# Kernel optimization log

Hardware: AMD Instinct MI355X
Metric: run time of the kernel (lower is better)

Reference implementation:

```python
import jax, jax.numpy as jnp
import numpy as np

E = 1024   # embedding_size
H = 16     # num_heads
DH = E // H


def setup_inputs() -> dict:
    key = jax.random.key(0)
    ks = jax.random.split(key, 11)
    B, S = 2, 2048
    std = 0.02
    return {
        "query": jax.random.normal(ks[0], (B, S, E), jnp.float32),
        "key": jax.random.normal(ks[1], (B, S, E), jnp.float32),
        "value": jax.random.normal(ks[2], (B, S, E), jnp.float32),
        "Wq": jax.random.normal(ks[3], (E, E), jnp.float32) * std,
        "bq": jnp.zeros((E,), jnp.float32),
        "Wk": jax.random.normal(ks[4], (E, E), jnp.float32) * std,
        "bk": jnp.zeros((E,), jnp.float32),
        "Wv": jax.random.normal(ks[5], (E, E), jnp.float32) * std,
        "bv": jnp.zeros((E,), jnp.float32),
        "Wo": jax.random.normal(ks[6], (E, E), jnp.float32) * std,
        "bo": jnp.zeros((E,), jnp.float32),
    }


def _split_heads(x, B, S):
    # [B,S,E] -> [B,H,S,DH]
    return x.reshape(B, S, H, DH).transpose(0, 2, 1, 3)


def reference(query, key, value, Wq, bq, Wk, bk, Wv, bv, Wo, bo):
    B, S, _ = query.shape
    # torch Linear: y = x @ W.T + b
    q = _split_heads(query @ Wq.T + bq, B, S)
    k = _split_heads(key @ Wk.T + bk, B, key.shape[1])
    v = _split_heads(value @ Wv.T + bv, B, value.shape[1])
    # naive unscaled attention (original has no 1/sqrt(d) factor)
    scores = jnp.einsum("bhsd,bhtd->bhst", q, k)  # [B,H,S,T]
    attn = jax.nn.softmax(scores, axis=-1)
    out = jnp.einsum("bhst,bhtd->bhsd", attn, v)  # [B,H,S,DH]
    out = out.transpose(0, 2, 1, 3).reshape(B, S, E)
    return out @ Wo.T + bo
```

## Files before the change

kernel.cpp:

```cpp
#include <hip/hip_runtime.h>
#include <hip/hip_bf16.h>

constexpr int kB   = 2;
constexpr int kS   = 2048;
constexpr int kE   = 1024;
constexpr int kH   = 16;
constexpr int kDH  = 64;
constexpr int kTok = kB * kS;

typedef short bf16x8 __attribute__((ext_vector_type(8)));
typedef float f32x4  __attribute__((ext_vector_type(4)));

__device__ __forceinline__ float bf2f(unsigned short s) {
  union { unsigned int u; float f; } c; c.u = ((unsigned int)s) << 16; return c.f;
}
__device__ __forceinline__ unsigned short f2bf(float f) {
  union { float f; unsigned int u; } c; c.f = f;
  unsigned int u = c.u;
  u += 0x7fffu + ((u >> 16) & 1u);
  return (unsigned short)(u >> 16);
}

__device__ __forceinline__ void gl_lds16(const unsigned short* g, unsigned short* l) {
  __builtin_amdgcn_global_load_lds(
      (const __attribute__((address_space(1))) unsigned int*)g,
      (__attribute__((address_space(3))) unsigned int*)l, 16, 0, 0);
}

__global__ void detect_dtype(const unsigned short* __restrict__ q, int* flag) {
  __shared__ int cnt;
  if (threadIdx.x == 0) cnt = 0;
  __syncthreads();
  int bad = 0;
  for (int i = threadIdx.x; i < 4096; i += 256) {
    unsigned int e = (q[i] >> 7) & 0xFF;
    if (e >= 0xC0) bad++;
  }
  atomicAdd(&cnt, bad);
  __syncthreads();
  if (threadIdx.x == 0) *flag = (cnt > 8) ? 1 : 0;
}

struct Seg { const void* src; unsigned short* dst; unsigned int n; unsigned int blk0; };
struct ConvArgs { Seg s[11]; };

__global__ __launch_bounds__(256) void conv_all(ConvArgs a, const int* __restrict__ flag) {
  const unsigned int bid = blockIdx.x;
  int si = 0;
  #pragma unroll
  for (int i = 1; i < 11; ++i)
    if (bid >= a.s[i].blk0) si = i;
  const Seg sg = a.s[si];
  const int i0 = ((int)(bid - sg.blk0) * 256 + threadIdx.x) * 8;
  if (i0 >= (int)sg.n) return;
  if (*flag) {
    const float* s = (const float*)sg.src + i0;
    f32x4 f0 = *(const f32x4*)(s);
    f32x4 f1 = *(const f32x4*)(s + 4);
    bf16x8 v;
    #pragma unroll
    for (int j = 0; j < 4; ++j) v[j]     = (short)f2bf(f0[j]);
    #pragma unroll
    for (int j = 0; j < 4; ++j) v[j + 4] = (short)f2bf(f1[j]);
    *(bf16x8*)&sg.dst[i0] = v;
  } else {
    *(bf16x8*)&sg.dst[i0] = *(const bf16x8*)((const unsigned short*)sg.src + i0);
  }
}

__device__ __forceinline__ void gemm_core(
    const unsigned short* __restrict__ A,
    const unsigned short* __restrict__ W,
    int Kdim, int bM, int bN,
    unsigned short* As, unsigned short* Ws,
    f32x4 acc[4][4])
{
  const int tid  = threadIdx.x;
  const int lane = tid & 63;
  const int wv   = tid >> 6;
  const int wm   = (wv >> 1) * 64;
  const int wn   = (wv & 1) * 64;
  const int lr   = lane & 15;
  const int kq   = (lane >> 4) * 8;

  const int r0 = tid >> 2;
  const int c0 = (tid & 3) * 8;

  const unsigned short* Ag = A + (size_t)(bM + r0) * Kdim + c0;
  const unsigned short* Wg = W + (size_t)(bN + r0) * Kdim + c0;
  unsigned short* lA = &As[tid * 8];
  unsigned short* lW = &Ws[tid * 8];

  for (int k0 = 0; k0 < Kdim; k0 += 32) {
    gl_lds16(Ag + k0,                      lA);
    gl_lds16(Ag + (size_t)64 * Kdim + k0,  lA + 2048);
    gl_lds16(Wg + k0,                      lW);
    gl_lds16(Wg + (size_t)64 * Kdim + k0,  lW + 2048);
    __syncthreads();

    bf16x8 a[4], b[4];
    #pragma unroll
    for (int i = 0; i < 4; ++i)
      a[i] = *(const bf16x8*)&As[(wm + i * 16 + lr) * 32 + kq];
    #pragma unroll
    for (int i = 0; i < 4; ++i)
      b[i] = *(const bf16x8*)&Ws[(wn + i * 16 + lr) * 32 + kq];
    #pragma unroll
    for (int i = 0; i < 4; ++i)
      #pragma unroll
      for (int j = 0; j < 4; ++j)
        acc[i][j] = __builtin_amdgcn_mfma_f32_16x16x32_bf16(a[i], b[j], acc[i][j], 0, 0, 0);
    __syncthreads();
  }
}

__global__ __launch_bounds__(256) void gemm_qkv(
    const unsigned short* __restrict__ Abase,
    const unsigned short* __restrict__ Wbase,
    const unsigned short* __restrict__ biasbase,
    unsigned short* __restrict__ Cbase)
{
  __shared__ unsigned short As[128 * 32];
  __shared__ unsigned short Ws[128 * 32];

  const int z = blockIdx.z;
  const unsigned short* A    = Abase    + (size_t)z * (kTok * kE);
  const unsigned short* W    = Wbase    + (size_t)z * (kE * kE);
  const unsigned short* bias = biasbase + (size_t)z * kE;
  unsigned short* C          = Cbase    + (size_t)z * (kTok * kE);

  const int bM = blockIdx.y * 128;
  const int bN = blockIdx.x * 128;

  f32x4 acc[4][4] = {};
  gemm_core(A, W, kE, bM, bN, As, Ws, acc);

  const int lane = threadIdx.x & 63;
  const int wv   = threadIdx.x >> 6;
  const int wm   = (wv >> 1) * 64;
  const int wn   = (wv & 1) * 64;
  const int lr   = lane & 15;
  const int qd   = lane >> 4;
  #pragma unroll
  for (int j = 0; j < 4; ++j) {
    const int col = bN + wn + j * 16 + lr;
    const float bb = bf2f(bias[col]);
    #pragma unroll
    for (int i = 0; i < 4; ++i)
      #pragma unroll
      for (int r = 0; r < 4; ++r) {
        const int row = bM + wm + i * 16 + qd * 4 + r;
        C[(size_t)row * kE + col] = f2bf(acc[i][j][r] + bb);
      }
  }
}

__global__ __launch_bounds__(256) void vtrans(
    const unsigned short* __restrict__ Vb,
    unsigned short* __restrict__ Vt)
{
  __shared__ unsigned short Lt[64 * 72];
  const int tid = threadIdx.x;
  const int bh  = blockIdx.y;
  const int b   = bh >> 4;
  const int h   = bh & 15;
  const int hcol = h * kDH;
  const int s0  = blockIdx.x * 64;

  #pragma unroll
  for (int issue = 0; issue < 2; ++issue) {
    int g = issue * 256 + tid;
    int r = g >> 3, c = (g & 7) * 8;
    bf16x8 vv = *(const bf16x8*)&Vb[(size_t)(b * kS + s0 + r) * kE + hcol + c];
    const int swz = ((((r >> 3) ^ (c >> 3)) & 7) << 3) + (r & 7);
    #pragma unroll
    for (int i = 0; i < 8; ++i)
      Lt[(c + i) * 72 + swz] = (unsigned short)vv[i];
  }
  __syncthreads();
  #pragma unroll
  for (int issue = 0; issue < 2; ++issue) {
    int g = issue * 256 + tid;
    int f = g >> 3, tc = (g & 7) * 8;
    const int blk = ((tc >> 3) ^ (f >> 3)) & 7;
    bf16x8 vv = *(const bf16x8*)&Lt[f * 72 + (blk << 3)];
    *(bf16x8*)&Vt[(size_t)b * (kE * kS) + (size_t)(hcol + f) * kS + s0 + tc] = vv;
  }
}

__global__ __launch_bounds__(256) void gemm_out(
    const unsigned short* __restrict__ A,
    const unsigned short* __restrict__ W,
    const unsigned short* __restrict__ bias,
    void* __restrict__ C,
    const int* __restrict__ flag)
{
  __shared__ unsigned short As[128 * 32];
  __shared__ unsigned short Ws[128 * 32];

  const int bM = blockIdx.y * 128;
  const int bN = blockIdx.x * 128;

  f32x4 acc[4][4] = {};
  gemm_core(A, W, kE, bM, bN, As, Ws, acc);

  const int lane = threadIdx.x & 63;
  const int wv   = threadIdx.x >> 6;
  const int wm   = (wv >> 1) * 64;
  const int wn   = (wv & 1) * 64;
  const int lr   = lane & 15;
  const int qd   = lane >> 4;
  if (*flag) {
    float* Cf = (float*)C;
    #pragma unroll
    for (int j = 0; j < 4; ++j) {
      const int col = bN + wn + j * 16 + lr;
      const float bb = bf2f(bias[col]);
      #pragma unroll
      for (int i = 0; i < 4; ++i)
        #pragma unroll
        for (int r = 0; r < 4; ++r) {
          const int row = bM + wm + i * 16 + qd * 4 + r;
          Cf[(size_t)row * kE + col] = acc[i][j][r] + bb;
        }
    }
  } else {
    unsigned short* Cb = (unsigned short*)C;
    #pragma unroll
    for (int j = 0; j < 4; ++j) {
      const int col = bN + wn + j * 16 + lr;
      const float bb = bf2f(bias[col]);
      #pragma unroll
      for (int i = 0; i < 4; ++i)
        #pragma unroll
        for (int r = 0; r < 4; ++r) {
          const int row = bM + wm + i * 16 + qd * 4 + r;
          Cb[(size_t)row * kE + col] = f2bf(acc[i][j][r] + bb);
        }
    }
  }
}

__global__ __launch_bounds__(256) void attn(
    const unsigned short* __restrict__ Qb,
    const unsigned short* __restrict__ Kb,
    const unsigned short* __restrict__ Vt,
    unsigned short* __restrict__ Ob)
{
  __shared__ unsigned short Qs[64 * 72];
  __shared__ unsigned short Ks[64 * 72];
  __shared__ unsigned short Vs[64 * 72];
  __shared__ unsigned short Ps[64 * 72];

  const int tid  = threadIdx.x;
  const int lane = tid & 63;
  const int w    = tid >> 6;
  const int lr   = lane & 15;
  const int quad = lane >> 4;
  const int kq   = quad * 8;

  const int bh = blockIdx.y;
  const int b  = bh >> 4;
  const int h  = bh & 15;
  const int q0 = blockIdx.x * 64;

  const size_t rowbase = (size_t)b * kS * kE;
  const int hcol = h * kDH;
  const unsigned short* Vbase = Vt + (size_t)b * (kE * kS) + (size_t)hcol * kS;

  const int r0 = tid >> 3;
  const int c0 = (tid & 7) * 8;

  #pragma unroll
  for (int issue = 0; issue < 2; ++issue) {
    int r = issue * 32 + r0;
    *(bf16x8*)&Qs[r * 72 + c0] =
        *(const bf16x8*)&Qb[rowbase + (size_t)(q0 + r) * kE + hcol + c0];
  }
  __syncthreads();

  const bf16x8 aq0 = *(const bf16x8*)&Qs[(w * 16 + lr) * 72 + 0 + kq];
  const bf16x8 aq1 = *(const bf16x8*)&Qs[(w * 16 + lr) * 72 + 32 + kq];

  f32x4 o[4] = {};
  float l_r[4] = {0.f, 0.f, 0.f, 0.f};

  bf16x8 rk0 = *(const bf16x8*)&Kb[rowbase + (size_t)(r0)      * kE + hcol + c0];
  bf16x8 rk1 = *(const bf16x8*)&Kb[rowbase + (size_t)(r0 + 32) * kE + hcol + c0];
  bf16x8 rv0 = *(const bf16x8*)&Vbase[(size_t)(r0)      * kS + c0];
  bf16x8 rv1 = *(const bf16x8*)&Vbase[(size_t)(r0 + 32) * kS + c0];

  for (int t0 = 0; t0 < kS; t0 += 64) {
    __syncthreads();
    *(bf16x8*)&Ks[ r0       * 72 + c0] = rk0;
    *(bf16x8*)&Ks[(r0 + 32) * 72 + c0] = rk1;
    *(bf16x8*)&Vs[ r0       * 72 + c0] = rv0;
    *(bf16x8*)&Vs[(r0 + 32) * 72 + c0] = rv1;
    __syncthreads();

    const int t1 = t0 + 64;
    if (t1 < kS) {
      rk0 = *(const bf16x8*)&Kb[rowbase + (size_t)(t1 + r0)      * kE + hcol + c0];
      rk1 = *(const bf16x8*)&Kb[rowbase + (size_t)(t1 + r0 + 32) * kE + hcol + c0];
      rv0 = *(const bf16x8*)&Vbase[(size_t)(r0)      * kS + t1 + c0];
      rv1 = *(const bf16x8*)&Vbase[(size_t)(r0 + 32) * kS + t1 + c0];
    }

    f32x4 s[4] = {};
    #pragma unroll
    for (int tn = 0; tn < 4; ++tn) {
      const bf16x8 bk0 = *(const bf16x8*)&Ks[(tn * 16 + lr) * 72 + 0 + kq];
      const bf16x8 bk1 = *(const bf16x8*)&Ks[(tn * 16 + lr) * 72 + 32 + kq];
      s[tn] = __builtin_amdgcn_mfma_f32_16x16x32_bf16(aq0, bk0, s[tn], 0, 0, 0);
      s[tn] = __builtin_amdgcn_mfma_f32_16x16x32_bf16(aq1, bk1, s[tn], 0, 0, 0);
    }

    #pragma unroll
    for (int tn = 0; tn < 4; ++tn)
      #pragma unroll
      for (int r = 0; r < 4; ++r) {
        const float p = __expf(s[tn][r]);
        l_r[r] += p;
        Ps[(w * 16 + quad * 4 + r) * 72 + ((tn ^ quad) << 4) + lr] = f2bf(p);
      }

    #pragma unroll
    for (int kk = 0; kk < 2; ++kk) {
      const int tnr = kk * 2 + (quad >> 1);
      const int tph = tnr ^ ((lr >> 2) & 3);
      const bf16x8 ap =
          *(const bf16x8*)&Ps[(w * 16 + lr) * 72 + (tph << 4) + ((quad & 1) << 3)];
      #pragma unroll
      for (int dt = 0; dt < 4; ++dt) {
        const bf16x8 bv = *(const bf16x8*)&Vs[(dt * 16 + lr) * 72 + kk * 32 + kq];
        o[dt] = __builtin_amdgcn_mfma_f32_16x16x32_bf16(ap, bv, o[dt], 0, 0, 0);
      }
    }
  }

  #pragma unroll
  for (int r = 0; r < 4; ++r) {
    #pragma unroll
    for (int off = 1; off < 16; off <<= 1)
      l_r[r] += __shfl_xor(l_r[r], off, 64);
  }

  #pragma unroll
  for (int dt = 0; dt < 4; ++dt) {
    #pragma unroll
    for (int r = 0; r < 4; ++r) {
      const int row = q0 + w * 16 + quad * 4 + r;
      const int col = hcol + dt * 16 + lr;
      Ob[rowbase + (size_t)row * kE + col] = f2bf(o[dt][r] / l_r[r]);
    }
  }
}

extern "C" void kernel_launch(void* const* d_in, const int* in_sizes, int n_in,
                              void* d_out, int out_size, void* d_ws, size_t ws_size,
                              hipStream_t stream) {
  const int nQKV = kTok * kE;
  const int nW   = kE * kE;
  const int nB   = kE;

  char* wsb = (char*)d_ws;
  int* flag = (int*)wsb;
  unsigned short* qc  = (unsigned short*)(wsb + 16);
  unsigned short* kc  = qc  + (size_t)nQKV;
  unsigned short* vc  = kc  + (size_t)nQKV;
  unsigned short* Wqc = vc  + (size_t)nQKV;
  unsigned short* Wkc = Wqc + (size_t)nW;
  unsigned short* Wvc = Wkc + (size_t)nW;
  unsigned short* Woc = Wvc + (size_t)nW;
  unsigned short* bqc = Woc + (size_t)nW;
  unsigned short* bkc = bqc + nB;
  unsigned short* bvc = bkc + nB;
  unsigned short* boc = bvc + nB;
  unsigned short* Qb  = boc + nB;
  unsigned short* Kb  = Qb  + (size_t)nQKV;
  unsigned short* Vb  = Kb  + (size_t)nQKV;
  unsigned short* Vtb = kc;
  unsigned short* Ob  = qc;

  detect_dtype<<<1, 256, 0, stream>>>((const unsigned short*)d_in[0], flag);

  ConvArgs ca;
  const void* srcs[11] = { d_in[0], d_in[1], d_in[2], d_in[3], d_in[4], d_in[5],
                           d_in[6], d_in[7], d_in[8], d_in[9], d_in[10] };
  unsigned short* dsts[11] = { qc, kc, vc, Wqc, bqc, Wkc, bkc, Wvc, bvc, Woc, boc };
  const unsigned int ns[11] = { (unsigned)nQKV, (unsigned)nQKV, (unsigned)nQKV,
                                (unsigned)nW, (unsigned)nB, (unsigned)nW, (unsigned)nB,
                                (unsigned)nW, (unsigned)nB, (unsigned)nW, (unsigned)nB };
  unsigned int blk = 0;
  for (int i = 0; i < 11; ++i) {
    ca.s[i].src = srcs[i]; ca.s[i].dst = dsts[i]; ca.s[i].n = ns[i]; ca.s[i].blk0 = blk;
    blk += (ns[i] + 2047) / 2048;
  }
  conv_all<<<blk, 256, 0, stream>>>(ca, flag);

  dim3 blk256(256);
  dim3 gqkv(kE / 128, kTok / 128, 3);
  gemm_qkv<<<gqkv, blk256, 0, stream>>>(qc, Wqc, bqc, Qb);

  dim3 gvt(kS / 64, kB * kH);
  vtrans<<<gvt, blk256, 0, stream>>>(Vb, Vtb);

  dim3 gattn(kS / 64, kB * kH);
  attn<<<gattn, blk256, 0, stream>>>(Qb, Kb, Vtb, Ob);

  dim3 gout(kE / 128, kTok / 128);
  gemm_out<<<gout, blk256, 0, stream>>>(Ob, Woc, boc, d_out, flag);
}
```

Measured before the change: 282.6 us.

## Keep attention probabilities in registers via transposed QK MFMA and permlane swaps

The QK^T MFMA operands are swapped so each lane holds scores transposed, and the P matrix is packed to bf16 with v_cvt_pk_bf16_f32 and rearranged with permlane32/permlane16 swaps into the A-operand layout for the PV MFMA. This removes the per-tile Ps shared-memory round trip (scalar bf16 stores plus vector loads) and its LDS footprint. The row-sum reduction is reworked to match the new layout, and the final normalisation uses a reciprocal multiply. It relies on gfx950 permlane swap instructions and on the lane mapping being exactly right.

```diff
diff --git a/kernel.cpp b/kernel.cpp
--- a/kernel.cpp
+++ b/kernel.cpp
@@ -10,6 +10,7 @@
 
 typedef short bf16x8 __attribute__((ext_vector_type(8)));
 typedef float f32x4  __attribute__((ext_vector_type(4)));
+typedef unsigned int uint2v __attribute__((ext_vector_type(2)));
 
 __device__ __forceinline__ float bf2f(unsigned short s) {
   union { unsigned int u; float f; } c; c.u = ((unsigned int)s) << 16; return c.f;
@@ -19,6 +20,12 @@
   unsigned int u = c.u;
   u += 0x7fffu + ((u >> 16) & 1u);
   return (unsigned short)(u >> 16);
+}
+
+__device__ __forceinline__ unsigned cvtpk(float lo, float hi) {
+  unsigned r;
+  asm("v_cvt_pk_bf16_f32 %0, %1, %2" : "=v"(r) : "v"(lo), "v"(hi));
+  return r;
 }
 
 __device__ __forceinline__ void gl_lds16(const unsigned short* g, unsigned short* l) {
@@ -250,7 +257,6 @@
   __shared__ unsigned short Qs[64 * 72];
   __shared__ unsigned short Ks[64 * 72];
   __shared__ unsigned short Vs[64 * 72];
-  __shared__ unsigned short Ps[64 * 72];
 
   const int tid  = threadIdx.x;
   const int lane = tid & 63;
@@ -283,7 +289,7 @@
   const bf16x8 aq1 = *(const bf16x8*)&Qs[(w * 16 + lr) * 72 + 32 + kq];
 
   f32x4 o[4] = {};
-  float l_r[4] = {0.f, 0.f, 0.f, 0.f};
+  float l4[4] = {0.f, 0.f, 0.f, 0.f};
 
   bf16x8 rk0 = *(const bf16x8*)&Kb[rowbase + (size_t)(r0)      * kE + hcol + c0];
   bf16x8 rk1 = *(const bf16x8*)&Kb[rowbase + (size_t)(r0 + 32) * kE + hcol + c0];
@@ -311,39 +317,54 @@
     for (int tn = 0; tn < 4; ++tn) {
       const bf16x8 bk0 = *(const bf16x8*)&Ks[(tn * 16 + lr) * 72 + 0 + kq];
       const bf16x8 bk1 = *(const bf16x8*)&Ks[(tn * 16 + lr) * 72 + 32 + kq];
-      s[tn] = __builtin_amdgcn_mfma_f32_16x16x32_bf16(aq0, bk0, s[tn], 0, 0, 0);
-      s[tn] = __builtin_amdgcn_mfma_f32_16x16x32_bf16(aq1, bk1, s[tn], 0, 0, 0);
-    }
-
+      s[tn] = __builtin_amdgcn_mfma_f32_16x16x32_bf16(bk0, aq0, s[tn], 0, 0, 0);
+      s[tn] = __builtin_amdgcn_mfma_f32_16x16x32_bf16(bk1, aq1, s[tn], 0, 0, 0);
+    }
+
+    float p[4][4];
     #pragma unroll
     for (int tn = 0; tn < 4; ++tn)
       #pragma unroll
       for (int r = 0; r < 4; ++r) {
-        const float p = __expf(s[tn][r]);
-        l_r[r] += p;
-        Ps[(w * 16 + quad * 4 + r) * 72 + ((tn ^ quad) << 4) + lr] = f2bf(p);
+        p[tn][r] = __expf(s[tn][r]);
+        l4[r] += p[tn][r];
       }
 
+    bf16x8 ap[2];
     #pragma unroll
     for (int kk = 0; kk < 2; ++kk) {
-      const int tnr = kk * 2 + (quad >> 1);
-      const int tph = tnr ^ ((lr >> 2) & 3);
-      const bf16x8 ap =
-          *(const bf16x8*)&Ps[(w * 16 + lr) * 72 + (tph << 4) + ((quad & 1) << 3)];
+      const unsigned A0 = cvtpk(p[2 * kk][0],     p[2 * kk][1]);
+      const unsigned A1 = cvtpk(p[2 * kk + 1][0], p[2 * kk + 1][1]);
+      const uint2v u   = __builtin_amdgcn_permlane32_swap(A0, A1, false, false);
+      const uint2v z02 = __builtin_amdgcn_permlane16_swap(u[0], u[1], false, false);
+      const unsigned B0 = cvtpk(p[2 * kk][2],     p[2 * kk][3]);
+      const unsigned B1 = cvtpk(p[2 * kk + 1][2], p[2 * kk + 1][3]);
+      const uint2v v2  = __builtin_amdgcn_permlane32_swap(B0, B1, false, false);
+      const uint2v z13 = __builtin_amdgcn_permlane16_swap(v2[0], v2[1], false, false);
+      union { unsigned ud[4]; bf16x8 v; } pk;
+      pk.ud[0] = z02[0];
+      pk.ud[1] = z13[0];
+      pk.ud[2] = z02[1];
+      pk.ud[3] = z13[1];
+      ap[kk] = pk.v;
+    }
+
+    #pragma unroll
+    for (int kk = 0; kk < 2; ++kk)
       #pragma unroll
       for (int dt = 0; dt < 4; ++dt) {
         const bf16x8 bv = *(const bf16x8*)&Vs[(dt * 16 + lr) * 72 + kk * 32 + kq];
-        o[dt] = __builtin_amdgcn_mfma_f32_16x16x32_bf16(ap, bv, o[dt], 0, 0, 0);
+        o[dt] = __builtin_amdgcn_mfma_f32_16x16x32_bf16(ap[kk], bv, o[dt], 0, 0, 0);
       }
-    }
-  }
-
-  #pragma unroll
-  for (int r = 0; r < 4; ++r) {
-    #pragma unroll
-    for (int off = 1; off < 16; off <<= 1)
-      l_r[r] += __shfl_xor(l_r[r], off, 64);
-  }
+  }
+
+  float l = (l4[0] + l4[1]) + (l4[2] + l4[3]);
+  l += __shfl_xor(l, 16, 64);
+  l += __shfl_xor(l, 32, 64);
+  float inv[4];
+  #pragma unroll
+  for (int r = 0; r < 4; ++r)
+    inv[r] = 1.0f / __shfl(l, quad * 4 + r, 64);
 
   #pragma unroll
   for (int dt = 0; dt < 4; ++dt) {
@@ -351,7 +372,7 @@
     for (int r = 0; r < 4; ++r) {
       const int row = q0 + w * 16 + quad * 4 + r;
       const int col = hcol + dt * 16 + lr;
-      Ob[rowbase + (size_t)row * kE + col] = f2bf(o[dt][r] / l_r[r]);
+      Ob[rowbase + (size_t)row * kE + col] = f2bf(o[dt][r] * inv[r]);
     }
   }
 }
```

After: 273.9 us. 1.03x faster.
